# Optimization experiments

Measured on AMD Instinct MI355X. Metric: run time of the kernel, lower is better.

## Reference

```python
import jax, jax.numpy as jnp
import numpy as np

NEG_SLOPE = 0.1  # leaky_relu slope used by Conv1dNormRelu in the repo


def grid_sample_bilinear(feat, xy):
    """Bilinear sample feat [B,C,H,W] at pixel coords xy [B,2,N].

    Equivalent to the repo's grid_sample_wrapper: it normalizes xy to [-1,1]
    and calls F.grid_sample(align_corners=True, padding_mode='zeros'), which
    maps back to exactly these pixel coordinates. Out-of-bounds corners -> 0.
    Returns [B,C,N].
    """
    B, C, H, W = feat.shape
    x = xy[:, 0]  # [B,N]
    y = xy[:, 1]
    x0 = jnp.floor(x)
    y0 = jnp.floor(y)
    wx1 = x - x0
    wy1 = y - y0
    wx0 = 1.0 - wx1
    wy0 = 1.0 - wy1

    def gather(ix, iy):
        valid = (ix >= 0) & (ix <= W - 1) & (iy >= 0) & (iy <= H - 1)
        ixc = jnp.clip(ix, 0, W - 1).astype(jnp.int32)
        iyc = jnp.clip(iy, 0, H - 1).astype(jnp.int32)
        # per-batch gather: f[:, iy, ix] -> [C, N]
        v = jax.vmap(lambda f, iy_, ix_: f[:, iy_, ix_])(feat, iyc, ixc)  # [B,C,N]
        return v * valid[:, None, :].astype(feat.dtype)

    out = (gather(x0, y0) * (wx0 * wy0)[:, None, :]
           + gather(x0 + 1, y0) * (wx1 * wy0)[:, None, :]
           + gather(x0, y0 + 1) * (wx0 * wy1)[:, None, :]
           + gather(x0 + 1, y0 + 1) * (wx1 * wy1)[:, None, :])
    return out


def setup_inputs() -> dict:
    key = jax.random.key(0)
    k1, k2, k3, k4 = jax.random.split(key, 4)
    B, N = 4, 16384
    C2D, C3D, H, W_img = 128, 128, 96, 160
    # pixel coords in [0, W-1] x [0, H-1]
    u = jax.random.uniform(k1, (B, 1, N), dtype=jnp.float32) * (W_img - 1)
    v = jax.random.uniform(k2, (B, 1, N), dtype=jnp.float32) * (H - 1)
    xy = jnp.concatenate([u, v], axis=1)  # [B,2,N]
    feat_2d = jax.random.normal(k3, (B, C2D, H, W_img), dtype=jnp.float32)
    feat_3d = jax.random.normal(k4, (B, C3D, N), dtype=jnp.float32)
    kw, kb = jax.random.split(jax.random.fold_in(key, 7))
    fan_in = C2D + C3D
    W = jax.random.normal(kw, (C3D, fan_in), dtype=jnp.float32) / np.sqrt(fan_in)
    b = jnp.zeros((C3D,), dtype=jnp.float32)
    return {"xy": xy, "feat_2d": feat_2d, "feat_3d": feat_3d, "W": W, "b": b}


def reference(xy, feat_2d, feat_3d, W, b):
    # torch.no_grad() around the gather -> stop_gradient
    feat_2d_to_3d = jax.lax.stop_gradient(grid_sample_bilinear(feat_2d, xy))  # [B,C2d,N]
    cat = jnp.concatenate([feat_2d_to_3d, feat_3d], axis=1)  # [B,C2d+C3d,N]
    # Conv1d with kernel_size=1 == pointwise matmul over channels
    y = jnp.einsum('oi,bin->bon', W, cat) + b[None, :, None]
    return jnp.where(y >= 0, y, NEG_SLOPE * y)
```

## Files before the change

kernel.cpp:

```cpp
#include <hip/hip_runtime.h>
#include <hip/hip_bf16.h>

#define NSAMP 16384
#define BB    4
#define C2D   128
#define C3D   128
#define HH    96
#define WW    160
#define COUT  128
#define KK    256
#define HW    (HH*WW)
#define TN    64
#define CATS  264
#define TS    136

typedef __attribute__((ext_vector_type(8))) short bf16x8;
typedef __attribute__((ext_vector_type(4))) float f32x4;

__device__ __forceinline__ float bf16lo(unsigned int u) { return __uint_as_float(u << 16); }
__device__ __forceinline__ float bf16hi(unsigned int u) { return __uint_as_float(u & 0xffff0000u); }
__device__ __forceinline__ unsigned int pack2(float a, float b) {
    union { __hip_bfloat162 h; unsigned int u; } c;
    c.h = __float22bfloat162_rn(make_float2(a, b));
    return c.u;
}

__global__ __launch_bounds__(256) void wcvt_kernel(
    const float* __restrict__ Wm, unsigned short* __restrict__ Wb)
{
    const int i = blockIdx.x * 256 + threadIdx.x;
    const float4 v = ((const float4*)Wm)[i];
    uint2 o;
    o.x = pack2(v.x, v.y);
    o.y = pack2(v.z, v.w);
    ((uint2*)Wb)[i] = o;
}

__global__ __launch_bounds__(512) void transpose_cvt_kernel(
    const float* __restrict__ f2d, unsigned short* __restrict__ f2dt)
{
    __shared__ unsigned short t[128 * TS];
    unsigned int* tw = (unsigned int*)t;
    const int tid  = threadIdx.x;
    const int lane = tid & 63;
    const int wv   = tid >> 6;
    const int blk  = (blockIdx.x & 7) * 60 + (blockIdx.x >> 3);
    const int b    = blk / 120;
    const int hw0  = (blk % 120) * 128;

    const int xk = 4 * ((lane >> 3) & 7);
    const float* src = f2d + (size_t)b * C2D * HW + hw0 + lane;
    #pragma unroll
    for (int st = 0; st < 8; ++st) {
        const int c = wv * 16 + st * 2;
        const float va0 = src[(size_t)c * HW];
        const float vb0 = src[(size_t)(c + 1) * HW];
        const float va1 = src[(size_t)c * HW + 64];
        const float vb1 = src[(size_t)(c + 1) * HW + 64];
        const int w = (c >> 1) ^ xk;
        tw[lane        * (TS / 2) + w] = pack2(va0, vb0);
        tw[(lane + 64) * (TS / 2) + w] = pack2(va1, vb1);
    }
    __syncthreads();
    #pragma unroll
    for (int it = 0; it < 4; ++it) {
        const int r  = it * 32 + (tid >> 4);
        const int rk = 4 * ((r >> 3) & 7);
        const uint4 v = *(const uint4*)&tw[r * (TS / 2) + (((tid & 15) * 4) ^ rk)];
        *(uint4*)&f2dt[((size_t)b * HW + hw0 + r) * C2D + (tid & 15) * 8] = v;
    }
}

__device__ __forceinline__ void blend_write(
    const uint2* cv, const float4 bw, unsigned int* catw, int row, int ch4)
{
    float r0 = bw.x * bf16lo(cv[0].x) + bw.y * bf16lo(cv[1].x)
             + bw.z * bf16lo(cv[2].x) + bw.w * bf16lo(cv[3].x);
    float r1 = bw.x * bf16hi(cv[0].x) + bw.y * bf16hi(cv[1].x)
             + bw.z * bf16hi(cv[2].x) + bw.w * bf16hi(cv[3].x);
    float r2 = bw.x * bf16lo(cv[0].y) + bw.y * bf16lo(cv[1].y)
             + bw.z * bf16lo(cv[2].y) + bw.w * bf16lo(cv[3].y);
    float r3 = bw.x * bf16hi(cv[0].y) + bw.y * bf16hi(cv[1].y)
             + bw.z * bf16hi(cv[2].y) + bw.w * bf16hi(cv[3].y);
    uint2 pk;
    pk.x = pack2(r0, r1);
    pk.y = pack2(r2, r3);
    *(uint2*)&catw[row * (CATS / 2) + (ch4 >> 1)] = pk;
}

__global__ __launch_bounds__(256, 4) void fuse_kernel(
    const float*          __restrict__ xy,
    const unsigned short* __restrict__ f2dt,
    const float*          __restrict__ f3d,
    const unsigned short* __restrict__ Wb,
    const float*          __restrict__ bias,
    float* __restrict__ out)
{
    __shared__ unsigned short cat[TN * CATS];
    __shared__ float4 sw4[TN];
    __shared__ int4   soff4[TN];
    unsigned int* catw = (unsigned int*)cat;

    const int tid  = threadIdx.x;
    const int lane = tid & 63;
    const int wv   = tid >> 6;
    const int blk  = (blockIdx.x & 7) * 128 + (blockIdx.x >> 3);
    const int b    = blk >> 8;
    const int n0   = (blk & 255) * TN;

    if (tid < TN) {
        const int n = n0 + tid;
        float x = xy[((size_t)b * 2 + 0) * NSAMP + n];
        float y = xy[((size_t)b * 2 + 1) * NSAMP + n];
        float xf = floorf(x), yf = floorf(y);
        float wx1 = x - xf, wy1 = y - yf;
        float wx0 = 1.0f - wx1, wy0 = 1.0f - wy1;
        int x0 = (int)xf, y0 = (int)yf;
        int x1 = x0 + 1, y1 = y0 + 1;
        if (x0 < 0 || x0 > WW - 1) wx0 = 0.0f;
        if (x1 < 0 || x1 > WW - 1) wx1 = 0.0f;
        if (y0 < 0 || y0 > HH - 1) wy0 = 0.0f;
        if (y1 < 0 || y1 > HH - 1) wy1 = 0.0f;
        x0 = min(max(x0, 0), WW - 1);
        x1 = min(max(x1, 0), WW - 1);
        y0 = min(max(y0, 0), HH - 1);
        y1 = min(max(y1, 0), HH - 1);
        sw4[tid]   = make_float4(wx0 * wy0, wx1 * wy0, wx0 * wy1, wx1 * wy1);
        soff4[tid] = make_int4(y0 * WW + x0, y0 * WW + x1,
                               y1 * WW + x0, y1 * WW + x1);
    }

    {
        const float* p3 = f3d + (size_t)(b * C3D) * NSAMP + n0 + lane;
        #pragma unroll
        for (int ch = 0; ch < 4; ++ch) {
            const int cbase = wv * 32 + ch * 8;
            float v[8];
            #pragma unroll
            for (int t = 0; t < 8; ++t) v[t] = p3[(size_t)(cbase + t) * NSAMP];
            uint4 pk;
            pk.x = pack2(v[0], v[1]);
            pk.y = pack2(v[2], v[3]);
            pk.z = pack2(v[4], v[5]);
            pk.w = pack2(v[6], v[7]);
            *(uint4*)&catw[lane * (CATS / 2) + (C2D / 2) + (cbase >> 1)] = pk;
        }
    }
    __syncthreads();

    const int quad = lane >> 4;
    const int nloc = lane & 15;
    const int s2   = lane >> 5;
    const int ch4  = (lane & 31) * 4;
    const unsigned short* fb = f2dt + (size_t)b * HW * C2D + ch4;

    uint2  ga[4][4];
    float4 wA[4];
    #pragma unroll
    for (int i = 0; i < 4; ++i) {
        const int j = wv * 16 + i * 2 + s2;
        const int4 o = soff4[j];
        wA[i] = sw4[j];
        ga[i][0] = *(const uint2*)(fb + (size_t)o.x * C2D);
        ga[i][1] = *(const uint2*)(fb + (size_t)o.y * C2D);
        ga[i][2] = *(const uint2*)(fb + (size_t)o.z * C2D);
        ga[i][3] = *(const uint2*)(fb + (size_t)o.w * C2D);
    }

    f32x4 acc[2][4];
    #pragma unroll
    for (int mt = 0; mt < 2; ++mt)
        #pragma unroll
        for (int nt = 0; nt < 4; ++nt)
            acc[mt][nt] = (f32x4){0.f, 0.f, 0.f, 0.f};

    const unsigned short* wb0 = Wb + (size_t)(wv * 32 + nloc) * KK + quad * 8;

    #pragma unroll
    for (int ks = 4; ks < 8; ++ks) {
        const int k0 = ks * 32;
        const bf16x8 a0 = *(const bf16x8*)(wb0 + k0);
        const bf16x8 a1 = *(const bf16x8*)(wb0 + 16 * KK + k0);
        #pragma unroll
        for (int nt = 0; nt < 4; ++nt) {
            const bf16x8 bfrag = *(const bf16x8*)
                &cat[(nt * 16 + nloc) * CATS + k0 + quad * 8];
            acc[0][nt] = __builtin_amdgcn_mfma_f32_16x16x32_bf16(
                a0, bfrag, acc[0][nt], 0, 0, 0);
            acc[1][nt] = __builtin_amdgcn_mfma_f32_16x16x32_bf16(
                a1, bfrag, acc[1][nt], 0, 0, 0);
        }
    }

    #pragma unroll
    for (int i = 0; i < 4; ++i) {
        const int j2 = wv * 16 + 8 + i * 2 + s2;
        const int4 o = soff4[j2];
        const float4 wv4 = sw4[j2];
        uint2 gb[4];
        gb[0] = *(const uint2*)(fb + (size_t)o.x * C2D);
        gb[1] = *(const uint2*)(fb + (size_t)o.y * C2D);
        gb[2] = *(const uint2*)(fb + (size_t)o.z * C2D);
        gb[3] = *(const uint2*)(fb + (size_t)o.w * C2D);
        blend_write(ga[i], wA[i], catw, wv * 16 + i * 2 + s2, ch4);
        blend_write(gb, wv4, catw, j2, ch4);
    }
    __syncthreads();

    #pragma unroll
    for (int ks = 0; ks < 4; ++ks) {
        const int k0 = ks * 32;
        const bf16x8 a0 = *(const bf16x8*)(wb0 + k0);
        const bf16x8 a1 = *(const bf16x8*)(wb0 + 16 * KK + k0);
        #pragma unroll
        for (int nt = 0; nt < 4; ++nt) {
            const bf16x8 bfrag = *(const bf16x8*)
                &cat[(nt * 16 + nloc) * CATS + k0 + quad * 8];
            acc[0][nt] = __builtin_amdgcn_mfma_f32_16x16x32_bf16(
                a0, bfrag, acc[0][nt], 0, 0, 0);
            acc[1][nt] = __builtin_amdgcn_mfma_f32_16x16x32_bf16(
                a1, bfrag, acc[1][nt], 0, 0, 0);
        }
    }

    #pragma unroll
    for (int mt = 0; mt < 2; ++mt) {
        const int cobase = wv * 32 + mt * 16 + quad * 4;
        float bv[4];
        #pragma unroll
        for (int r = 0; r < 4; ++r) bv[r] = bias[cobase + r];
        #pragma unroll
        for (int nt = 0; nt < 4; ++nt) {
            float* po = out + (size_t)(b * COUT + cobase) * NSAMP
                      + n0 + nt * 16 + nloc;
            #pragma unroll
            for (int r = 0; r < 4; ++r) {
                float yv = acc[mt][nt][r] + bv[r];
                yv = (yv >= 0.0f) ? yv : 0.1f * yv;
                po[(size_t)r * NSAMP] = yv;
            }
        }
    }
}

extern "C" void kernel_launch(void* const* d_in, const int* in_sizes, int n_in,
                              void* d_out, int out_size, void* d_ws, size_t ws_size,
                              hipStream_t stream) {
    const float* xy   = (const float*)d_in[0];
    const float* f2d  = (const float*)d_in[1];
    const float* f3d  = (const float*)d_in[2];
    const float* Wm   = (const float*)d_in[3];
    const float* bias = (const float*)d_in[4];
    float* out = (float*)d_out;

    unsigned short* f2dt = (unsigned short*)d_ws;
    unsigned short* Wb   = f2dt + (size_t)BB * HW * C2D;

    wcvt_kernel<<<dim3((COUT * KK / 4) / 256), 256, 0, stream>>>(Wm, Wb);
    transpose_cvt_kernel<<<dim3(BB * (HW / 128)), 512, 0, stream>>>(f2d, f2dt);
    fuse_kernel<<<dim3(BB * (NSAMP / TN)), 256, 0, stream>>>(
        xy, f2dt, f3d, Wb, bias, out);
}
```

Measured before the change: 128.8 us.

## Merge weight conversion into transpose kernel and issue all gathers before the GEMM

The separate weight-conversion launch is folded into the transpose kernel as 16 extra blocks, saving one kernel launch. In the fused kernel, each wave now computes the bilinear offsets and weights itself and passes them between lanes with shuffles instead of through shared memory. All gather loads are issued early so they overlap the f3d loads, then a single barrier is followed by one K loop. This drops the split-K overlap of half the MFMA work with the second gather batch, and holding more registers for gathers in flight may lower occupancy.

```diff
diff --git a/kernel.cpp b/kernel.cpp
--- a/kernel.cpp
+++ b/kernel.cpp
@@ -25,26 +25,26 @@
     return c.u;
 }
 
-__global__ __launch_bounds__(256) void wcvt_kernel(
-    const float* __restrict__ Wm, unsigned short* __restrict__ Wb)
-{
-    const int i = blockIdx.x * 256 + threadIdx.x;
-    const float4 v = ((const float4*)Wm)[i];
-    uint2 o;
-    o.x = pack2(v.x, v.y);
-    o.y = pack2(v.z, v.w);
-    ((uint2*)Wb)[i] = o;
-}
-
 __global__ __launch_bounds__(512) void transpose_cvt_kernel(
-    const float* __restrict__ f2d, unsigned short* __restrict__ f2dt)
+    const float* __restrict__ f2d, unsigned short* __restrict__ f2dt,
+    const float* __restrict__ Wm,  unsigned short* __restrict__ Wb)
 {
     __shared__ unsigned short t[128 * TS];
+    const int raw = blockIdx.x;
+    if (raw >= 480) {
+        const int i = (raw - 480) * 512 + threadIdx.x;
+        const float4 v = ((const float4*)Wm)[i];
+        uint2 o;
+        o.x = pack2(v.x, v.y);
+        o.y = pack2(v.z, v.w);
+        ((uint2*)Wb)[i] = o;
+        return;
+    }
     unsigned int* tw = (unsigned int*)t;
     const int tid  = threadIdx.x;
     const int lane = tid & 63;
     const int wv   = tid >> 6;
-    const int blk  = (blockIdx.x & 7) * 60 + (blockIdx.x >> 3);
+    const int blk  = (raw & 7) * 60 + (raw >> 3);
     const int b    = blk / 120;
     const int hw0  = (blk % 120) * 128;
 
@@ -97,8 +97,6 @@
     float* __restrict__ out)
 {
     __shared__ unsigned short cat[TN * CATS];
-    __shared__ float4 sw4[TN];
-    __shared__ int4   soff4[TN];
     unsigned int* catw = (unsigned int*)cat;
 
     const int tid  = threadIdx.x;
@@ -108,8 +106,10 @@
     const int b    = blk >> 8;
     const int n0   = (blk & 255) * TN;
 
-    if (tid < TN) {
-        const int n = n0 + tid;
+    float w4x, w4y, w4z, w4w;
+    int   o4x, o4y, o4z, o4w;
+    {
+        const int n = n0 + wv * 16 + (lane & 15);
         float x = xy[((size_t)b * 2 + 0) * NSAMP + n];
         float y = xy[((size_t)b * 2 + 1) * NSAMP + n];
         float xf = floorf(x), yf = floorf(y);
@@ -125,9 +125,26 @@
         x1 = min(max(x1, 0), WW - 1);
         y0 = min(max(y0, 0), HH - 1);
         y1 = min(max(y1, 0), HH - 1);
-        sw4[tid]   = make_float4(wx0 * wy0, wx1 * wy0, wx0 * wy1, wx1 * wy1);
-        soff4[tid] = make_int4(y0 * WW + x0, y0 * WW + x1,
-                               y1 * WW + x0, y1 * WW + x1);
+        w4x = wx0 * wy0; w4y = wx1 * wy0; w4z = wx0 * wy1; w4w = wx1 * wy1;
+        o4x = y0 * WW + x0; o4y = y0 * WW + x1;
+        o4z = y1 * WW + x0; o4w = y1 * WW + x1;
+    }
+
+    const int s2  = lane >> 5;
+    const int ch4 = (lane & 31) * 4;
+    const unsigned short* fb = f2dt + (size_t)b * HW * C2D + ch4;
+
+    uint2 ga[4][4];
+    #pragma unroll
+    for (int i = 0; i < 4; ++i) {
+        const int jl = i * 2 + s2;
+        int4 o;
+        o.x = __shfl(o4x, jl); o.y = __shfl(o4y, jl);
+        o.z = __shfl(o4z, jl); o.w = __shfl(o4w, jl);
+        ga[i][0] = *(const uint2*)(fb + (size_t)o.x * C2D);
+        ga[i][1] = *(const uint2*)(fb + (size_t)o.y * C2D);
+        ga[i][2] = *(const uint2*)(fb + (size_t)o.z * C2D);
+        ga[i][3] = *(const uint2*)(fb + (size_t)o.w * C2D);
     }
 
     {
@@ -146,26 +163,40 @@
             *(uint4*)&catw[lane * (CATS / 2) + (C2D / 2) + (cbase >> 1)] = pk;
         }
     }
+
+    uint2 gb[4][4];
+    #pragma unroll
+    for (int i = 0; i < 4; ++i) {
+        const int jl = 8 + i * 2 + s2;
+        int4 o;
+        o.x = __shfl(o4x, jl); o.y = __shfl(o4y, jl);
+        o.z = __shfl(o4z, jl); o.w = __shfl(o4w, jl);
+        gb[i][0] = *(const uint2*)(fb + (size_t)o.x * C2D);
+        gb[i][1] = *(const uint2*)(fb + (size_t)o.y * C2D);
+        gb[i][2] = *(const uint2*)(fb + (size_t)o.z * C2D);
+        gb[i][3] = *(const uint2*)(fb + (size_t)o.w * C2D);
+    }
+
+    #pragma unroll
+    for (int i = 0; i < 4; ++i) {
+        const int jl = i * 2 + s2;
+        float4 bw;
+        bw.x = __shfl(w4x, jl); bw.y = __shfl(w4y, jl);
+        bw.z = __shfl(w4z, jl); bw.w = __shfl(w4w, jl);
+        blend_write(ga[i], bw, catw, wv * 16 + jl, ch4);
+    }
+    #pragma unroll
+    for (int i = 0; i < 4; ++i) {
+        const int jl = 8 + i * 2 + s2;
+        float4 bw;
+        bw.x = __shfl(w4x, jl); bw.y = __shfl(w4y, jl);
+        bw.z = __shfl(w4z, jl); bw.w = __shfl(w4w, jl);
+        blend_write(gb[i], bw, catw, wv * 16 + jl, ch4);
+    }
     __syncthreads();
 
     const int quad = lane >> 4;
     const int nloc = lane & 15;
-    const int s2   = lane >> 5;
-    const int ch4  = (lane & 31) * 4;
-    const unsigned short* fb = f2dt + (size_t)b * HW * C2D + ch4;
-
-    uint2  ga[4][4];
-    float4 wA[4];
-    #pragma unroll
-    for (int i = 0; i < 4; ++i) {
-        const int j = wv * 16 + i * 2 + s2;
-        const int4 o = soff4[j];
-        wA[i] = sw4[j];
-        ga[i][0] = *(const uint2*)(fb + (size_t)o.x * C2D);
-        ga[i][1] = *(const uint2*)(fb + (size_t)o.y * C2D);
-        ga[i][2] = *(const uint2*)(fb + (size_t)o.z * C2D);
-        ga[i][3] = *(const uint2*)(fb + (size_t)o.w * C2D);
-    }
 
     f32x4 acc[2][4];
     #pragma unroll
@@ -176,39 +207,8 @@
 
     const unsigned short* wb0 = Wb + (size_t)(wv * 32 + nloc) * KK + quad * 8;
 
-    #pragma unroll
-    for (int ks = 4; ks < 8; ++ks) {
-        const int k0 = ks * 32;
-        const bf16x8 a0 = *(const bf16x8*)(wb0 + k0);
-        const bf16x8 a1 = *(const bf16x8*)(wb0 + 16 * KK + k0);
-        #pragma unroll
-        for (int nt = 0; nt < 4; ++nt) {
-            const bf16x8 bfrag = *(const bf16x8*)
-                &cat[(nt * 16 + nloc) * CATS + k0 + quad * 8];
-            acc[0][nt] = __builtin_amdgcn_mfma_f32_16x16x32_bf16(
-                a0, bfrag, acc[0][nt], 0, 0, 0);
-            acc[1][nt] = __builtin_amdgcn_mfma_f32_16x16x32_bf16(
-                a1, bfrag, acc[1][nt], 0, 0, 0);
-        }
-    }
-
-    #pragma unroll
-    for (int i = 0; i < 4; ++i) {
-        const int j2 = wv * 16 + 8 + i * 2 + s2;
-        const int4 o = soff4[j2];
-        const float4 wv4 = sw4[j2];
-        uint2 gb[4];
-        gb[0] = *(const uint2*)(fb + (size_t)o.x * C2D);
-        gb[1] = *(const uint2*)(fb + (size_t)o.y * C2D);
-        gb[2] = *(const uint2*)(fb + (size_t)o.z * C2D);
-        gb[3] = *(const uint2*)(fb + (size_t)o.w * C2D);
-        blend_write(ga[i], wA[i], catw, wv * 16 + i * 2 + s2, ch4);
-        blend_write(gb, wv4, catw, j2, ch4);
-    }
-    __syncthreads();
-
-    #pragma unroll
-    for (int ks = 0; ks < 4; ++ks) {
+    #pragma unroll 2
+    for (int ks = 0; ks < 8; ++ks) {
         const int k0 = ks * 32;
         const bf16x8 a0 = *(const bf16x8*)(wb0 + k0);
         const bf16x8 a1 = *(const bf16x8*)(wb0 + 16 * KK + k0);
@@ -256,8 +256,7 @@
     unsigned short* f2dt = (unsigned short*)d_ws;
     unsigned short* Wb   = f2dt + (size_t)BB * HW * C2D;
 
-    wcvt_kernel<<<dim3((COUT * KK / 4) / 256), 256, 0, stream>>>(Wm, Wb);
-    transpose_cvt_kernel<<<dim3(BB * (HW / 128)), 512, 0, stream>>>(f2d, f2dt);
+    transpose_cvt_kernel<<<dim3(496), 512, 0, stream>>>(f2d, f2dt, Wm, Wb);
     fuse_kernel<<<dim3(BB * (NSAMP / TN)), 256, 0, stream>>>(
         xy, f2dt, f3d, Wb, bias, out);
 }
```

Result: faster. 126.2 us (-2.0%).
